# Optimization experiments

Measured on AMD Instinct MI355X. Metric: run time of the kernel, lower is better.

The kernel has to match this reference:

```python
import jax, jax.numpy as jnp
import numpy as np

N, E, D, G, L, ED = 20000, 640000, 128, 128, 5, 7
BN_EPS = 1e-5


def _bn(x, g, b):
    # training-mode BatchNorm1d: biased batch statistics
    m = x.mean(axis=0)
    v = jnp.mean((x - m) ** 2, axis=0)
    return g * (x - m) / jnp.sqrt(v + BN_EPS) + b


def setup_inputs() -> dict:
    key = jax.random.key(0)
    ks = jax.random.split(key, 16)
    s = 0.05
    p = {}
    p["x"] = jax.random.normal(ks[0], (N, D), jnp.float32)
    p["edge_attr"] = jax.random.normal(ks[1], (E, ED), jnp.float32)
    p["edge_index"] = jax.random.randint(ks[2], (2, E), 0, N, jnp.int32)
    p["batch"] = jnp.sort(jax.random.randint(ks[3], (N,), 0, G, jnp.int32))
    p["enc_W"] = jax.random.normal(ks[4], (D, D), jnp.float32) * s
    p["enc_b"] = jnp.zeros((D,), jnp.float32)
    p["vn_emb"] = jnp.zeros((1, D), jnp.float32)  # init.constant_(0)
    p["eps"] = jnp.zeros((L,), jnp.float32)       # GIN eps init 0
    p["edge_W"] = jax.random.normal(ks[5], (L, ED, D), jnp.float32) * s
    p["edge_b"] = jnp.zeros((L, D), jnp.float32)
    p["mlp_W1"] = jax.random.normal(ks[6], (L, D, 2 * D), jnp.float32) * s
    p["mlp_b1"] = jnp.zeros((L, 2 * D), jnp.float32)
    p["mlp_bn1_g"] = jnp.ones((L, 2 * D), jnp.float32)
    p["mlp_bn1_b"] = jnp.zeros((L, 2 * D), jnp.float32)
    p["mlp_W2"] = jax.random.normal(ks[7], (L, 2 * D, D), jnp.float32) * s
    p["mlp_b2"] = jnp.zeros((L, D), jnp.float32)
    p["bn_g"] = jnp.ones((L, D), jnp.float32)
    p["bn_b"] = jnp.zeros((L, D), jnp.float32)
    p["vn_W1"] = jax.random.normal(ks[8], (L - 1, D, 2 * D), jnp.float32) * s
    p["vn_b1"] = jnp.zeros((L - 1, 2 * D), jnp.float32)
    p["vn_bn1_g"] = jnp.ones((L - 1, 2 * D), jnp.float32)
    p["vn_bn1_b"] = jnp.zeros((L - 1, 2 * D), jnp.float32)
    p["vn_W2"] = jax.random.normal(ks[9], (L - 1, 2 * D, D), jnp.float32) * s
    p["vn_b2"] = jnp.zeros((L - 1, D), jnp.float32)
    p["vn_bn2_g"] = jnp.ones((L - 1, D), jnp.float32)
    p["vn_bn2_b"] = jnp.zeros((L - 1, D), jnp.float32)
    return p


def reference(x, edge_attr, edge_index, batch, enc_W, enc_b, vn_emb, eps,
              edge_W, edge_b, mlp_W1, mlp_b1, mlp_bn1_g, mlp_bn1_b, mlp_W2,
              mlp_b2, bn_g, bn_b, vn_W1, vn_b1, vn_bn1_g, vn_bn1_b, vn_W2,
              vn_b2, vn_bn2_g, vn_bn2_b):
    src, dst = edge_index[0], edge_index[1]
    h = x @ enc_W + enc_b                       # node_encoder (Linear)
    vn = jnp.broadcast_to(vn_emb[0], (G, D))    # virtual node per graph, init 0
    for l in range(L):
        h_in = h + vn[batch]                    # gather virtual node into nodes
        # GINConv: message = relu(x_j + edge_emb), aggr='add'
        eemb = edge_attr @ edge_W[l] + edge_b[l]            # [E, D]
        msg = jax.nn.relu(h_in[src] + eemb)                 # [E, D]
        agg = jax.ops.segment_sum(msg, dst, num_segments=N) # scatter-add
        z = (1.0 + eps[l]) * h_in + agg
        z = jax.nn.relu(_bn(z @ mlp_W1[l] + mlp_b1[l], mlp_bn1_g[l], mlp_bn1_b[l]))
        z = z @ mlp_W2[l] + mlp_b2[l]
        hn = _bn(z, bn_g[l], bn_b[l])           # outer BatchNorm1d
        if l < L - 1:
            hn = jax.nn.relu(hn)                # relu on all but last layer
            # virtual node update: global_add_pool over h_list[layer] (= h_in)
            pooled = jax.ops.segment_sum(h_in, batch, num_segments=G) + vn
            t = jax.nn.relu(_bn(pooled @ vn_W1[l] + vn_b1[l], vn_bn1_g[l], vn_bn1_b[l]))
            vn = jax.nn.relu(_bn(t @ vn_W2[l] + vn_b2[l], vn_bn2_g[l], vn_bn2_b[l]))
        h = hn
    return h  # JK='last' node representation [N, D]
```

## Files before the change

kernel.cpp:

```cpp
#include <hip/hip_runtime.h>

#define N_NODES 20000
#define N_EDGES 640000
#define DIM 128
#define NGRAPH 128
#define NLAYER 5
#define EDIM 7
#define TWO_D 256

typedef __bf16 bf16x8 __attribute__((ext_vector_type(8)));
typedef __bf16 bf16x4 __attribute__((ext_vector_type(4)));
typedef __bf16 bf16x2 __attribute__((ext_vector_type(2)));
typedef float  f32x4  __attribute__((ext_vector_type(4)));

__device__ __forceinline__ f32x4 mfma16(bf16x8 a, bf16x8 b, f32x4 c) {
  return __builtin_amdgcn_mfma_f32_16x16x32_bf16(a, b, c, 0, 0, 0);
}

__global__ void k_hist(const int* __restrict__ dst, int* __restrict__ counts) {
  int e = blockIdx.x * blockDim.x + threadIdx.x;
  if (e < N_EDGES) atomicAdd(&counts[dst[e]], 1);
}

__global__ __launch_bounds__(1024) void k_scanA(const int* __restrict__ counts,
    int* __restrict__ local, int* __restrict__ bsum) {
  __shared__ int sd[1024];
  int b = blockIdx.x, tid = threadIdx.x;
  int i = b * 1024 + tid;
  int v = (i < N_NODES) ? counts[i] : 0;
  sd[tid] = v;
  __syncthreads();
  for (int ofs = 1; ofs < 1024; ofs <<= 1) {
    int t = (tid >= ofs) ? sd[tid - ofs] : 0;
    __syncthreads();
    sd[tid] += t;
    __syncthreads();
  }
  if (i <= N_NODES) local[i] = sd[tid] - v;
  if (tid == 1023) bsum[b] = sd[1023];
}

__global__ void k_scanB(int* __restrict__ bsum, int* __restrict__ carry,
                        int* __restrict__ offsets, const int* __restrict__ batch,
                        int* __restrict__ gs) {
  int tid = threadIdx.x;
  if (tid == 0) {
    int run = 0;
    for (int b = 0; b < 20; ++b) { carry[b] = run; run += bsum[b]; }
    offsets[N_NODES] = run;
  }
  if (tid <= NGRAPH) {
    if (tid == NGRAPH) gs[NGRAPH] = N_NODES;
    else {
      int lo = 0, hi = N_NODES;
      while (lo < hi) { int mid = (lo + hi) >> 1; if (batch[mid] < tid) lo = mid + 1; else hi = mid; }
      gs[tid] = lo;
    }
  }
}

__global__ __launch_bounds__(1024) void k_scanC(const int* __restrict__ local,
    const int* __restrict__ carry, int* __restrict__ offsets) {
  int i = blockIdx.x * 1024 + threadIdx.x;
  if (i < N_NODES) offsets[i] = local[i] + carry[i >> 10];
}

__global__ void k_fillA(const int* __restrict__ dstArr, const int* __restrict__ offsets,
                        int* __restrict__ cursor, int* __restrict__ perm) {
  int e = blockIdx.x * blockDim.x + threadIdx.x;
  if (e >= N_EDGES) return;
  int d = dstArr[e];
  int p = offsets[d] + atomicAdd(&cursor[d], 1);
  perm[p] = e;
}

__global__ void k_fillB(const int* __restrict__ perm, const int* __restrict__ srcArr,
                        const float* __restrict__ edge_attr,
                        int* __restrict__ csr_src, __bf16* __restrict__ ea_csr) {
  int i = blockIdx.x * blockDim.x + threadIdx.x;
  if (i >= N_EDGES) return;
  int e = perm[i];
  csr_src[i] = srcArr[e];
  const float* ea = edge_attr + (size_t)e * EDIM;
  bf16x8 v;
#pragma unroll
  for (int k = 0; k < EDIM; ++k) v[k] = (__bf16)ea[k];
  v[7] = (__bf16)0.f;
  *(bf16x8*)(ea_csr + (size_t)i * 8) = v;
}

__global__ void k_convAll(const float* __restrict__ encW, const float* __restrict__ W1,
    const float* __restrict__ W2,
    __bf16* __restrict__ encT_hi, __bf16* __restrict__ encT_lo,
    __bf16* __restrict__ W1T_hi, __bf16* __restrict__ W1T_lo,
    __bf16* __restrict__ W2T_hi, __bf16* __restrict__ W2T_lo) {
  const int t1 = DIM * DIM;
  const int t2 = NLAYER * DIM * TWO_D;
  const int total = t1 + t2 + t2;
  for (int i = blockIdx.x * blockDim.x + threadIdx.x; i < total;
       i += gridDim.x * blockDim.x) {
    const float* src; __bf16 *dh, *dl; int K, C, idx;
    if (i < t1)            { src = encW; dh = encT_hi; dl = encT_lo; K = DIM;   C = DIM;   idx = i; }
    else if (i < t1 + t2)  { src = W1;   dh = W1T_hi;  dl = W1T_lo;  K = DIM;   C = TWO_D; idx = i - t1; }
    else                   { src = W2;   dh = W2T_hi;  dl = W2T_lo;  K = TWO_D; C = DIM;   idx = i - t1 - t2; }
    int l = idx / (K * C);
    int rem = idx - l * K * C;
    int k = rem / C;
    int c = rem - k * C;
    float v = src[idx];
    __bf16 hi = (__bf16)v;
    __bf16 lo = (__bf16)(v - (float)hi);
    size_t o = (size_t)l * K * C + (size_t)c * K + k;
    dh[o] = hi;
    dl[o] = lo;
  }
}

__global__ void k_vninit(const float* __restrict__ vn_emb, float* __restrict__ vn) {
  int i = blockIdx.x * blockDim.x + threadIdx.x;
  if (i < NGRAPH * DIM) vn[i] = vn_emb[i & (DIM - 1)];
}

__global__ __launch_bounds__(128) void k_enc(const float* __restrict__ x,
    const __bf16* __restrict__ encT_hi, const __bf16* __restrict__ encT_lo,
    const float* __restrict__ enc_b, const float* __restrict__ vn_emb,
    __bf16* __restrict__ h_hi, __bf16* __restrict__ h_lo) {
  int lane = threadIdx.x & 63, wid = threadIdx.x >> 6;
  int rbase = blockIdx.x * 32 + wid * 16;
  int r = rbase + (lane & 15);
  int ko = (lane >> 4) * 8;
  const float* xr = x + (size_t)r * DIM;
  bf16x8 a_hi[4], a_lo[4];
#pragma unroll
  for (int ks = 0; ks < 4; ++ks) {
    f32x4 v0 = *(const f32x4*)(xr + ks * 32 + ko);
    f32x4 v1 = *(const f32x4*)(xr + ks * 32 + ko + 4);
    bf16x8 th, tl;
#pragma unroll
    for (int j = 0; j < 4; ++j) {
      th[j] = (__bf16)v0[j];     tl[j] = (__bf16)(v0[j] - (float)th[j]);
      th[4+j] = (__bf16)v1[j];   tl[4+j] = (__bf16)(v1[j] - (float)th[4+j]);
    }
    a_hi[ks] = th; a_lo[ks] = tl;
  }
  const f32x4 fz = {0.f, 0.f, 0.f, 0.f};
  f32x4 acc[8];
#pragma unroll
  for (int nf = 0; nf < 8; ++nf) acc[nf] = fz;
#pragma unroll
  for (int nf = 0; nf < 8; ++nf) {
    size_t wrow = (size_t)(nf * 16 + (lane & 15)) * DIM + ko;
    const __bf16* bh = encT_hi + wrow;
    const __bf16* bl = encT_lo + wrow;
#pragma unroll
    for (int ks = 0; ks < 4; ++ks) {
      bf16x8 wh = *(const bf16x8*)(bh + ks * 32);
      bf16x8 wl = *(const bf16x8*)(bl + ks * 32);
      acc[nf] = mfma16(a_hi[ks], wh, acc[nf]);
      acc[nf] = mfma16(a_lo[ks], wh, acc[nf]);
      acc[nf] = mfma16(a_hi[ks], wl, acc[nf]);
    }
  }
  int c0 = lane & 15;
  int rr = rbase + (lane >> 4) * 4;
#pragma unroll
  for (int nf = 0; nf < 8; ++nf) {
    int c = nf * 16 + c0;
    float bias = enc_b[c] + vn_emb[c];
#pragma unroll
    for (int j = 0; j < 4; ++j) {
      float v = acc[nf][j] + bias;
      __bf16 hi = (__bf16)v;
      h_hi[(size_t)(rr + j) * DIM + c] = hi;
      h_lo[(size_t)(rr + j) * DIM + c] = (__bf16)(v - (float)hi);
    }
  }
}

__global__ __launch_bounds__(1024) void k_pool(const __bf16* __restrict__ h_hi,
    const int* __restrict__ gs, const float* __restrict__ vnbuf,
    const float* __restrict__ vnr, const float* __restrict__ sv2,
    const float* __restrict__ qv2, const float* __restrict__ bn2g,
    const float* __restrict__ bn2b, int use_stats,
    float* __restrict__ pooled) {
  __shared__ float red[8][DIM];
  __shared__ float vns[DIM];
  int tid = threadIdx.x;
  int g = blockIdx.x;
  if (tid < DIM) {
    if (use_stats) {
      float s = 0.f, q = 0.f;
#pragma unroll
      for (int rep = 0; rep < 8; ++rep) { s += sv2[rep * DIM + tid]; q += qv2[rep * DIM + tid]; }
      float m = s * (1.f / NGRAPH);
      float var = q * (1.f / NGRAPH) - m * m;
      float a = bn2g[tid] / sqrtf(var + 1e-5f);
      vns[tid] = fmaxf(vnr[g * DIM + tid] * a + (bn2b[tid] - m * a), 0.f);
    } else {
      vns[tid] = vnbuf[g * DIM + tid];
    }
  }
  __syncthreads();
  int d = tid & 127, slot = tid >> 7;
  int lo = gs[g], hi = gs[g + 1];
  float acc = 0.f;
  for (int n = lo + slot; n < hi; n += 8)
    acc += (float)h_hi[(size_t)n * DIM + d];
  red[slot][d] = acc;
  __syncthreads();
  if (slot == 0) {
    float t = vns[d];
#pragma unroll
    for (int s2 = 0; s2 < 8; ++s2) t += red[s2][d];
    pooled[g * DIM + d] = t;
  }
}

__global__ __launch_bounds__(256) void k_agg(const __bf16* __restrict__ h_hi,
    const __bf16* __restrict__ h_lo, const int* __restrict__ offsets,
    const int* __restrict__ csr_src, const __bf16* __restrict__ ea_csr,
    const float* __restrict__ eW, const float* __restrict__ eB,
    const float* __restrict__ eps, int l,
    __bf16* __restrict__ z_hi, __bf16* __restrict__ z_lo) {
  int tid = threadIdx.x;
  int lane = tid & 63, w = tid >> 6;
  int l2 = lane * 2;
  int n = blockIdx.x * 4 + w;
  float w0[EDIM], w1[EDIM];
#pragma unroll
  for (int k = 0; k < EDIM; ++k) {
    float2 wv = *(const float2*)(eW + k * DIM + l2);
    w0[k] = wv.x; w1[k] = wv.y;
  }
  float2 ebv = *(const float2*)(eB + l2);
  int off = offsets[n], end = offsets[n + 1];
  float acc0 = 0.f, acc1 = 0.f;

  auto edge = [&](int iu) {
    int s = csr_src[iu];
    const unsigned* eu = (const unsigned*)(ea_csr + (size_t)iu * 8);
    unsigned u0 = eu[0], u1 = eu[1], u2 = eu[2], u3 = eu[3];
    unsigned hv = *(const unsigned*)(h_hi + (size_t)s * DIM + l2);
    float e0 = __builtin_bit_cast(float, u0 << 16);
    float e1 = __builtin_bit_cast(float, u0 & 0xffff0000u);
    float e2 = __builtin_bit_cast(float, u1 << 16);
    float e3 = __builtin_bit_cast(float, u1 & 0xffff0000u);
    float e4 = __builtin_bit_cast(float, u2 << 16);
    float e5 = __builtin_bit_cast(float, u2 & 0xffff0000u);
    float e6 = __builtin_bit_cast(float, u3 << 16);
    float m0 = __builtin_bit_cast(float, hv << 16) + ebv.x;
    float m1 = __builtin_bit_cast(float, hv & 0xffff0000u) + ebv.y;
    m0 = fmaf(e0, w0[0], m0); m1 = fmaf(e0, w1[0], m1);
    m0 = fmaf(e1, w0[1], m0); m1 = fmaf(e1, w1[1], m1);
    m0 = fmaf(e2, w0[2], m0); m1 = fmaf(e2, w1[2], m1);
    m0 = fmaf(e3, w0[3], m0); m1 = fmaf(e3, w1[3], m1);
    m0 = fmaf(e4, w0[4], m0); m1 = fmaf(e4, w1[4], m1);
    m0 = fmaf(e5, w0[5], m0); m1 = fmaf(e5, w1[5], m1);
    m0 = fmaf(e6, w0[6], m0); m1 = fmaf(e6, w1[6], m1);
    acc0 += fmaxf(m0, 0.f);
    acc1 += fmaxf(m1, 0.f);
  };

  int i = off;
  for (; i + 3 < end; i += 4) {
    int iu = __builtin_amdgcn_readfirstlane(i);
    edge(iu);
    edge(iu + 1);
    edge(iu + 2);
    edge(iu + 3);
  }
  for (; i < end; ++i) {
    edge(__builtin_amdgcn_readfirstlane(i));
  }
  float epsv = 1.f + eps[l];
  unsigned hvh = *(const unsigned*)(h_hi + (size_t)n * DIM + l2);
  unsigned hvl = *(const unsigned*)(h_lo + (size_t)n * DIM + l2);
  float s0 = __builtin_bit_cast(float, hvh << 16) + __builtin_bit_cast(float, hvl << 16);
  float s1 = __builtin_bit_cast(float, hvh & 0xffff0000u) + __builtin_bit_cast(float, hvl & 0xffff0000u);
  float v0 = epsv * s0 + acc0;
  float v1 = epsv * s1 + acc1;
  __bf16 hi0 = (__bf16)v0, hi1 = (__bf16)v1;
  bf16x2 zh; zh[0] = hi0; zh[1] = hi1;
  bf16x2 zl; zl[0] = (__bf16)(v0 - (float)hi0); zl[1] = (__bf16)(v1 - (float)hi1);
  *(bf16x2*)(z_hi + (size_t)n * DIM + l2) = zh;
  *(bf16x2*)(z_lo + (size_t)n * DIM + l2) = zl;
}

__global__ __launch_bounds__(256) void k_gemm1(const __bf16* __restrict__ z_hi,
    const __bf16* __restrict__ z_lo,
    const __bf16* __restrict__ W1T_hi, const __bf16* __restrict__ W1T_lo,
    const float* __restrict__ b1,
    __bf16* __restrict__ y1h, __bf16* __restrict__ y1l,
    float* __restrict__ s1, float* __restrict__ q1) {
  int tid = threadIdx.x;
  int lane = tid & 63, wid = tid >> 6;
  int rowH = wid >> 1, colH = wid & 1;
  int rbase = blockIdx.x * 32 + rowH * 16;
  int r = rbase + (lane & 15);
  int ko = (lane >> 4) * 8;
  bf16x8 a_hi[4], a_lo[4];
#pragma unroll
  for (int ks = 0; ks < 4; ++ks) {
    a_hi[ks] = *(const bf16x8*)(z_hi + (size_t)r * DIM + ks * 32 + ko);
    a_lo[ks] = *(const bf16x8*)(z_lo + (size_t)r * DIM + ks * 32 + ko);
  }
  const f32x4 fz = {0.f, 0.f, 0.f, 0.f};
  f32x4 acc[8];
#pragma unroll
  for (int nf8 = 0; nf8 < 8; ++nf8) acc[nf8] = fz;
#pragma unroll
  for (int nf8 = 0; nf8 < 8; ++nf8) {
    int nf = colH * 8 + nf8;
    size_t wrow = (size_t)(nf * 16 + (lane & 15)) * DIM + ko;
    const __bf16* bh = W1T_hi + wrow;
    const __bf16* bl = W1T_lo + wrow;
#pragma unroll
    for (int ks = 0; ks < 4; ++ks) {
      bf16x8 wh = *(const bf16x8*)(bh + ks * 32);
      bf16x8 wl = *(const bf16x8*)(bl + ks * 32);
      acc[nf8] = mfma16(a_hi[ks], wh, acc[nf8]);
      acc[nf8] = mfma16(a_lo[ks], wh, acc[nf8]);
      acc[nf8] = mfma16(a_hi[ks], wl, acc[nf8]);
    }
  }
  int c0 = lane & 15;
  int rr = rbase + (lane >> 4) * 4;
  int rep = blockIdx.x & 7;
#pragma unroll
  for (int nf8 = 0; nf8 < 8; ++nf8) {
    int c = (colH * 8 + nf8) * 16 + c0;
    float bias = b1[c];
    float s = 0.f, q = 0.f;
#pragma unroll
    for (int j = 0; j < 4; ++j) {
      float v = acc[nf8][j] + bias;
      __bf16 hi = (__bf16)v;
      y1h[(size_t)(rr + j) * TWO_D + c] = hi;
      y1l[(size_t)(rr + j) * TWO_D + c] = (__bf16)(v - (float)hi);
      s += v; q += v * v;
    }
    s += __shfl_xor(s, 16); s += __shfl_xor(s, 32);
    q += __shfl_xor(q, 16); q += __shfl_xor(q, 32);
    if (lane < 16) {
      atomicAdd(&s1[rep * TWO_D + c], s);
      atomicAdd(&q1[rep * TWO_D + c], q);
    }
  }
}

__global__ __launch_bounds__(256) void k_gemm2(const __bf16* __restrict__ y1h,
    const __bf16* __restrict__ y1l,
    const __bf16* __restrict__ W2T_hi, const __bf16* __restrict__ W2T_lo,
    const float* __restrict__ b2,
    const float* __restrict__ s1, const float* __restrict__ q1,
    const float* __restrict__ bn1g, const float* __restrict__ bn1b,
    float* __restrict__ y2, float* __restrict__ s2, float* __restrict__ q2) {
  __shared__ float sc1s[TWO_D], sh1s[TWO_D];
  int tid = threadIdx.x;
  {
    int c = tid;
    float s = 0.f, q = 0.f;
#pragma unroll
    for (int rep = 0; rep < 8; ++rep) { s += s1[rep * TWO_D + c]; q += q1[rep * TWO_D + c]; }
    float m = s * (1.f / N_NODES);
    float var = q * (1.f / N_NODES) - m * m;
    float a = bn1g[c] / sqrtf(var + 1e-5f);
    sc1s[c] = a; sh1s[c] = bn1b[c] - m * a;
  }
  __syncthreads();
  int lane = tid & 63, wid = tid >> 6;
  int rowH = wid >> 1, colH = wid & 1;
  int rbase = blockIdx.x * 32 + rowH * 16;
  int r = rbase + (lane & 15);
  int ko = (lane >> 4) * 8;
  bf16x8 a_hi[8], a_lo[8];
#pragma unroll
  for (int ks = 0; ks < 8; ++ks) {
    int kb = ks * 32 + ko;
    bf16x8 rh = *(const bf16x8*)(y1h + (size_t)r * TWO_D + kb);
    bf16x8 rl = *(const bf16x8*)(y1l + (size_t)r * TWO_D + kb);
    f32x4 sc0 = *(const f32x4*)(&sc1s[kb]);
    f32x4 sc1 = *(const f32x4*)(&sc1s[kb + 4]);
    f32x4 sh0 = *(const f32x4*)(&sh1s[kb]);
    f32x4 sh1 = *(const f32x4*)(&sh1s[kb + 4]);
    bf16x8 th, tl;
#pragma unroll
    for (int j = 0; j < 4; ++j) {
      float r0 = (float)rh[j] + (float)rl[j];
      float r1 = (float)rh[4 + j] + (float)rl[4 + j];
      float v0 = fmaxf(r0 * sc0[j] + sh0[j], 0.f);
      float v1 = fmaxf(r1 * sc1[j] + sh1[j], 0.f);
      th[j] = (__bf16)v0;     tl[j] = (__bf16)(v0 - (float)th[j]);
      th[4+j] = (__bf16)v1;   tl[4+j] = (__bf16)(v1 - (float)th[4+j]);
    }
    a_hi[ks] = th; a_lo[ks] = tl;
  }
  const f32x4 fz = {0.f, 0.f, 0.f, 0.f};
  f32x4 acc[4];
#pragma unroll
  for (int nf4 = 0; nf4 < 4; ++nf4) acc[nf4] = fz;
#pragma unroll
  for (int nf4 = 0; nf4 < 4; ++nf4) {
    int nf = colH * 4 + nf4;
    size_t wrow = (size_t)(nf * 16 + (lane & 15)) * TWO_D + ko;
    const __bf16* bh = W2T_hi + wrow;
    const __bf16* bl = W2T_lo + wrow;
#pragma unroll
    for (int ks = 0; ks < 8; ++ks) {
      bf16x8 wh = *(const bf16x8*)(bh + ks * 32);
      bf16x8 wl = *(const bf16x8*)(bl + ks * 32);
      acc[nf4] = mfma16(a_hi[ks], wh, acc[nf4]);
      acc[nf4] = mfma16(a_lo[ks], wh, acc[nf4]);
      acc[nf4] = mfma16(a_hi[ks], wl, acc[nf4]);
    }
  }
  int c0 = lane & 15;
  int rr = rbase + (lane >> 4) * 4;
  int rep = blockIdx.x & 7;
#pragma unroll
  for (int nf4 = 0; nf4 < 4; ++nf4) {
    int c = (colH * 4 + nf4) * 16 + c0;
    float bias = b2[c];
    float s = 0.f, q = 0.f;
#pragma unroll
    for (int j = 0; j < 4; ++j) {
      float v = acc[nf4][j] + bias;
      y2[(size_t)(rr + j) * DIM + c] = v;
      s += v; q += v * v;
    }
    s += __shfl_xor(s, 16); s += __shfl_xor(s, 32);
    q += __shfl_xor(q, 16); q += __shfl_xor(q, 32);
    if (lane < 16) {
      atomicAdd(&s2[rep * DIM + c], s);
      atomicAdd(&q2[rep * DIM + c], q);
    }
  }
}

__global__ __launch_bounds__(256) void k_vgemm1(const float* __restrict__ pooled,
    const float* __restrict__ W1, const float* __restrict__ b1,
    float* __restrict__ tv, float* __restrict__ sv1, float* __restrict__ qv1) {
  __shared__ float row[DIM];
  int g = blockIdx.x, tid = threadIdx.x;
  if (tid < DIM) row[tid] = pooled[g * DIM + tid];
  __syncthreads();
  int c = tid;
  float acc = b1[c];
  for (int k = 0; k < DIM; ++k) acc = fmaf(row[k], W1[k * TWO_D + c], acc);
  tv[g * TWO_D + c] = acc;
  int rep = g & 7;
  atomicAdd(&sv1[rep * TWO_D + c], acc);
  atomicAdd(&qv1[rep * TWO_D + c], acc * acc);
}

__global__ __launch_bounds__(256) void k_vgemm2(const float* __restrict__ tv,
    const float* __restrict__ sv1, const float* __restrict__ qv1,
    const float* __restrict__ bn1g, const float* __restrict__ bn1b,
    const float* __restrict__ W2, const float* __restrict__ b2,
    float* __restrict__ vnr, float* __restrict__ sv2, float* __restrict__ qv2) {
  __shared__ float trow[TWO_D];
  int g = blockIdx.x, tid = threadIdx.x;
  {
    float s = 0.f, q = 0.f;
#pragma unroll
    for (int rep = 0; rep < 8; ++rep) { s += sv1[rep * TWO_D + tid]; q += qv1[rep * TWO_D + tid]; }
    float m = s * (1.f / NGRAPH);
    float var = q * (1.f / NGRAPH) - m * m;
    float a = bn1g[tid] / sqrtf(var + 1e-5f);
    trow[tid] = fmaxf(tv[g * TWO_D + tid] * a + (bn1b[tid] - m * a), 0.f);
  }
  __syncthreads();
  if (tid < DIM) {
    float acc = b2[tid];
    for (int k = 0; k < TWO_D; ++k) acc = fmaf(trow[k], W2[k * DIM + tid], acc);
    vnr[g * DIM + tid] = acc;
    int rep = g & 7;
    atomicAdd(&sv2[rep * DIM + tid], acc);
    atomicAdd(&qv2[rep * DIM + tid], acc * acc);
  }
}

__global__ __launch_bounds__(256) void k_bn2hin(const float* __restrict__ y2,
    const float* __restrict__ s2, const float* __restrict__ q2,
    const float* __restrict__ bng, const float* __restrict__ bnb,
    const float* __restrict__ vnr, const float* __restrict__ sv2,
    const float* __restrict__ qv2, const float* __restrict__ vbn2g,
    const float* __restrict__ vbn2b, const int* __restrict__ batch,
    __bf16* __restrict__ h_hi, __bf16* __restrict__ h_lo) {
  __shared__ float sc2s[DIM], sh2s[DIM], scvn[DIM], shvn[DIM];
  int tid = threadIdx.x;
  if (tid < DIM) {
    float s = 0.f, q = 0.f;
#pragma unroll
    for (int rep = 0; rep < 8; ++rep) { s += s2[rep * DIM + tid]; q += q2[rep * DIM + tid]; }
    float m = s * (1.f / N_NODES);
    float var = q * (1.f / N_NODES) - m * m;
    float a = bng[tid] / sqrtf(var + 1e-5f);
    sc2s[tid] = a; sh2s[tid] = bnb[tid] - m * a;
    float sv = 0.f, qv = 0.f;
#pragma unroll
    for (int rep = 0; rep < 8; ++rep) { sv += sv2[rep * DIM + tid]; qv += qv2[rep * DIM + tid]; }
    float mv = sv * (1.f / NGRAPH);
    float varv = qv * (1.f / NGRAPH) - mv * mv;
    float av = vbn2g[tid] / sqrtf(varv + 1e-5f);
    scvn[tid] = av; shvn[tid] = vbn2b[tid] - mv * av;
  }
  __syncthreads();
  int idx = blockIdx.x * 256 + tid;
  if (idx >= N_NODES * (DIM / 4)) return;
  int c4 = idx & 31;
  int row = idx >> 5;
  f32x4 y = ((const f32x4*)y2)[idx];
  f32x4 scv = ((const f32x4*)sc2s)[c4];
  f32x4 shv = ((const f32x4*)sh2s)[c4];
  f32x4 vsc = ((const f32x4*)scvn)[c4];
  f32x4 vsh = ((const f32x4*)shvn)[c4];
  int b = batch[row];
  f32x4 vr = ((const f32x4*)vnr)[b * 32 + c4];
  bf16x4 oh, ol;
#pragma unroll
  for (int j = 0; j < 4; ++j) {
    float vnv = fmaxf(vr[j] * vsc[j] + vsh[j], 0.f);
    float o = fmaxf(y[j] * scv[j] + shv[j], 0.f) + vnv;
    __bf16 hi = (__bf16)o;
    oh[j] = hi;
    ol[j] = (__bf16)(o - (float)hi);
  }
  ((bf16x4*)h_hi)[idx] = oh;
  ((bf16x4*)h_lo)[idx] = ol;
}

__global__ __launch_bounds__(256) void k_out(const float* __restrict__ y2,
    const float* __restrict__ s2, const float* __restrict__ q2,
    const float* __restrict__ bng, const float* __restrict__ bnb,
    float* __restrict__ out) {
  __shared__ float sc2s[DIM], sh2s[DIM];
  int tid = threadIdx.x;
  if (tid < DIM) {
    float s = 0.f, q = 0.f;
#pragma unroll
    for (int rep = 0; rep < 8; ++rep) { s += s2[rep * DIM + tid]; q += q2[rep * DIM + tid]; }
    float m = s * (1.f / N_NODES);
    float var = q * (1.f / N_NODES) - m * m;
    float a = bng[tid] / sqrtf(var + 1e-5f);
    sc2s[tid] = a; sh2s[tid] = bnb[tid] - m * a;
  }
  __syncthreads();
  int idx = blockIdx.x * 256 + tid;
  if (idx >= N_NODES * (DIM / 4)) return;
  int c4 = idx & 31;
  f32x4 y = ((const f32x4*)y2)[idx];
  f32x4 scv = ((const f32x4*)sc2s)[c4];
  f32x4 shv = ((const f32x4*)sh2s)[c4];
  f32x4 o;
#pragma unroll
  for (int j = 0; j < 4; ++j) o[j] = y[j] * scv[j] + shv[j];
  ((f32x4*)out)[idx] = o;
}

extern "C" void kernel_launch(void* const* d_in, const int* in_sizes, int n_in,
                              void* d_out, int out_size, void* d_ws, size_t ws_size,
                              hipStream_t stream) {
  const float* x         = (const float*)d_in[0];
  const float* edge_attr = (const float*)d_in[1];
  const int*   edge_index= (const int*)d_in[2];
  const int*   batch     = (const int*)d_in[3];
  const float* enc_W     = (const float*)d_in[4];
  const float* enc_b     = (const float*)d_in[5];
  const float* vn_emb    = (const float*)d_in[6];
  const float* eps       = (const float*)d_in[7];
  const float* edge_W    = (const float*)d_in[8];
  const float* edge_b    = (const float*)d_in[9];
  const float* mlp_W1    = (const float*)d_in[10];
  const float* mlp_b1    = (const float*)d_in[11];
  const float* mlp_bn1_g = (const float*)d_in[12];
  const float* mlp_bn1_b = (const float*)d_in[13];
  const float* mlp_W2    = (const float*)d_in[14];
  const float* mlp_b2    = (const float*)d_in[15];
  const float* bn_g      = (const float*)d_in[16];
  const float* bn_b      = (const float*)d_in[17];
  const float* vn_W1     = (const float*)d_in[18];
  const float* vn_b1     = (const float*)d_in[19];
  const float* vn_bn1_g  = (const float*)d_in[20];
  const float* vn_bn1_b  = (const float*)d_in[21];
  const float* vn_W2     = (const float*)d_in[22];
  const float* vn_b2     = (const float*)d_in[23];
  const float* vn_bn2_g  = (const float*)d_in[24];
  const float* vn_bn2_b  = (const float*)d_in[25];

  char* wsb = (char*)d_ws;
  size_t off = 0;
  auto take = [&](size_t bytes) -> void* {
    void* p = wsb + off;
    off += (bytes + 255) & ~(size_t)255;
    return p;
  };
  int*    counts  = (int*)take((size_t)2 * N_NODES * 4);
  int*    cursor  = counts + N_NODES;
  float*  stats   = (float*)take((size_t)NLAYER * 12288 * 4);
  __bf16* h_hi    = (__bf16*)take((size_t)N_NODES * DIM * 2);
  __bf16* h_lo    = (__bf16*)take((size_t)N_NODES * DIM * 2);
  float*  y2      = (float*)take((size_t)N_NODES * DIM * 4);
  __bf16* y1h     = (__bf16*)take((size_t)N_NODES * TWO_D * 2);
  __bf16* y1l     = (__bf16*)take((size_t)N_NODES * TWO_D * 2);
  __bf16* z_hi    = (__bf16*)take((size_t)N_NODES * DIM * 2);
  __bf16* z_lo    = (__bf16*)take((size_t)N_NODES * DIM * 2);
  int*    csr_src = (int*)take((size_t)N_EDGES * 4);
  __bf16* ea_csr  = (__bf16*)take((size_t)N_EDGES * 8 * 2);
  int*    perm    = (int*)take((size_t)N_EDGES * 4);
  int*    offsets = (int*)take((size_t)(N_NODES + 1) * 4);
  int*    slocal  = (int*)take((size_t)(N_NODES + 1024) * 4);
  int*    sbsum   = (int*)take(64 * 4);
  int*    scarry  = sbsum + 32;
  int*    gs      = (int*)take((size_t)(NGRAPH + 1) * 4);
  float*  pooled  = (float*)take((size_t)NGRAPH * DIM * 4);
  float*  tv      = (float*)take((size_t)NGRAPH * TWO_D * 4);
  float*  vnr     = (float*)take((size_t)NGRAPH * DIM * 4);
  float*  vn0     = (float*)take((size_t)NGRAPH * DIM * 4);
  __bf16* encT_hi = (__bf16*)take((size_t)DIM * DIM * 2);
  __bf16* encT_lo = (__bf16*)take((size_t)DIM * DIM * 2);
  __bf16* W1T_hi  = (__bf16*)take((size_t)NLAYER * DIM * TWO_D * 2);
  __bf16* W1T_lo  = (__bf16*)take((size_t)NLAYER * DIM * TWO_D * 2);
  __bf16* W2T_hi  = (__bf16*)take((size_t)NLAYER * TWO_D * DIM * 2);
  __bf16* W2T_lo  = (__bf16*)take((size_t)NLAYER * TWO_D * DIM * 2);
  if (off > ws_size) return;

  const int* srcArr = edge_index;
  const int* dstArr = edge_index + N_EDGES;

  hipMemsetAsync(counts, 0, (size_t)2 * N_NODES * 4 + (size_t)NLAYER * 12288 * 4, stream);

  k_hist<<<N_EDGES / 256, 256, 0, stream>>>(dstArr, counts);
  k_scanA<<<20, 1024, 0, stream>>>(counts, slocal, sbsum);
  k_scanB<<<1, 256, 0, stream>>>(sbsum, scarry, offsets, batch, gs);
  k_scanC<<<20, 1024, 0, stream>>>(slocal, scarry, offsets);
  k_fillA<<<N_EDGES / 256, 256, 0, stream>>>(dstArr, offsets, cursor, perm);
  k_fillB<<<N_EDGES / 256, 256, 0, stream>>>(perm, srcArr, edge_attr, csr_src, ea_csr);
  k_convAll<<<336, 1024, 0, stream>>>(enc_W, mlp_W1, mlp_W2,
      encT_hi, encT_lo, W1T_hi, W1T_lo, W2T_hi, W2T_lo);
  k_vninit<<<(NGRAPH * DIM) / 256, 256, 0, stream>>>(vn_emb, vn0);
  k_enc<<<N_NODES / 32, 128, 0, stream>>>(x, encT_hi, encT_lo, enc_b, vn_emb, h_hi, h_lo);

  for (int l = 0; l < NLAYER; ++l) {
    float* s1  = stats + (size_t)l * 12288;
    float* q1  = s1 + 2048;
    float* s2  = s1 + 4096;
    float* q2  = s1 + 5120;
    float* sv1 = s1 + 6144;
    float* qv1 = s1 + 8192;
    float* sv2 = s1 + 10240;
    float* qv2 = s1 + 11264;
    if (l < NLAYER - 1) {
      if (l == 0)
        k_pool<<<NGRAPH, 1024, 0, stream>>>(h_hi, gs, vn0, vn0, nullptr, nullptr,
            nullptr, nullptr, 0, pooled);
      else {
        float* psv2 = stats + (size_t)(l - 1) * 12288 + 10240;
        float* pqv2 = stats + (size_t)(l - 1) * 12288 + 11264;
        k_pool<<<NGRAPH, 1024, 0, stream>>>(h_hi, gs, vn0, vnr, psv2, pqv2,
            vn_bn2_g + (size_t)(l - 1) * DIM, vn_bn2_b + (size_t)(l - 1) * DIM, 1, pooled);
      }
    }
    k_agg<<<N_NODES / 4, 256, 0, stream>>>(h_hi, h_lo, offsets, csr_src, ea_csr,
        edge_W + (size_t)l * EDIM * DIM, edge_b + (size_t)l * DIM, eps, l, z_hi, z_lo);
    k_gemm1<<<N_NODES / 32, 256, 0, stream>>>(z_hi, z_lo,
        W1T_hi + (size_t)l * DIM * TWO_D, W1T_lo + (size_t)l * DIM * TWO_D,
        mlp_b1 + (size_t)l * TWO_D, y1h, y1l, s1, q1);
    k_gemm2<<<N_NODES / 32, 256, 0, stream>>>(y1h, y1l,
        W2T_hi + (size_t)l * TWO_D * DIM, W2T_lo + (size_t)l * TWO_D * DIM,
        mlp_b2 + (size_t)l * DIM, s1, q1,
        mlp_bn1_g + (size_t)l * TWO_D, mlp_bn1_b + (size_t)l * TWO_D,
        y2, s2, q2);
    if (l < NLAYER - 1) {
      k_vgemm1<<<NGRAPH, 256, 0, stream>>>(pooled, vn_W1 + (size_t)l * DIM * TWO_D,
          vn_b1 + (size_t)l * TWO_D, tv, sv1, qv1);
      k_vgemm2<<<NGRAPH, 256, 0, stream>>>(tv, sv1, qv1,
          vn_bn1_g + (size_t)l * TWO_D, vn_bn1_b + (size_t)l * TWO_D,
          vn_W2 + (size_t)l * TWO_D * DIM, vn_b2 + (size_t)l * DIM,
          vnr, sv2, qv2);
      k_bn2hin<<<(N_NODES * 32) / 256, 256, 0, stream>>>(y2, s2, q2,
          bn_g + (size_t)l * DIM, bn_b + (size_t)l * DIM,
          vnr, sv2, qv2, vn_bn2_g + (size_t)l * DIM, vn_bn2_b + (size_t)l * DIM,
          batch, h_hi, h_lo);
    } else {
      k_out<<<(N_NODES * 32) / 256, 256, 0, stream>>>(y2, s2, q2,
          bn_g + (size_t)l * DIM, bn_b + (size_t)l * DIM, (float*)d_out);
    }
  }
}
```

Before: 740.5 us.

## Fuse graph pooling into producer kernels via atomics; process two nodes per wave in agg

Removes the separate k_pool and k_vninit kernels. Per-graph sums of h_in are now accumulated with float atomics into 8 replicated partial buffers inside k_enc and k_bn2hin, and the virtual-node term is added in k_vgemm1. k_agg now handles two destination nodes per wave with interleaved edge loops, which adds memory-level parallelism. The price is many atomic adds (one per element, into 8 replicas), a larger memset of the pooled buffers, and nondeterministic float summation order. Pooling now sums the fp32 value rather than only the bf16 hi part.

```diff
diff --git a/kernel.cpp b/kernel.cpp
--- a/kernel.cpp
+++ b/kernel.cpp
@@ -116,15 +116,12 @@
   }
 }
 
-__global__ void k_vninit(const float* __restrict__ vn_emb, float* __restrict__ vn) {
-  int i = blockIdx.x * blockDim.x + threadIdx.x;
-  if (i < NGRAPH * DIM) vn[i] = vn_emb[i & (DIM - 1)];
-}
-
 __global__ __launch_bounds__(128) void k_enc(const float* __restrict__ x,
     const __bf16* __restrict__ encT_hi, const __bf16* __restrict__ encT_lo,
     const float* __restrict__ enc_b, const float* __restrict__ vn_emb,
-    __bf16* __restrict__ h_hi, __bf16* __restrict__ h_lo) {
+    const int* __restrict__ batch,
+    __bf16* __restrict__ h_hi, __bf16* __restrict__ h_lo,
+    float* __restrict__ pooled0) {
   int lane = threadIdx.x & 63, wid = threadIdx.x >> 6;
   int rbase = blockIdx.x * 32 + wid * 16;
   int r = rbase + (lane & 15);
@@ -163,6 +160,10 @@
   }
   int c0 = lane & 15;
   int rr = rbase + (lane >> 4) * 4;
+  int bj[4];
+#pragma unroll
+  for (int j = 0; j < 4; ++j) bj[j] = batch[rr + j];
+  float* prep = pooled0 + (size_t)(blockIdx.x & 7) * NGRAPH * DIM;
 #pragma unroll
   for (int nf = 0; nf < 8; ++nf) {
     int c = nf * 16 + c0;
@@ -173,46 +174,8 @@
       __bf16 hi = (__bf16)v;
       h_hi[(size_t)(rr + j) * DIM + c] = hi;
       h_lo[(size_t)(rr + j) * DIM + c] = (__bf16)(v - (float)hi);
-    }
-  }
-}
-
-__global__ __launch_bounds__(1024) void k_pool(const __bf16* __restrict__ h_hi,
-    const int* __restrict__ gs, const float* __restrict__ vnbuf,
-    const float* __restrict__ vnr, const float* __restrict__ sv2,
-    const float* __restrict__ qv2, const float* __restrict__ bn2g,
-    const float* __restrict__ bn2b, int use_stats,
-    float* __restrict__ pooled) {
-  __shared__ float red[8][DIM];
-  __shared__ float vns[DIM];
-  int tid = threadIdx.x;
-  int g = blockIdx.x;
-  if (tid < DIM) {
-    if (use_stats) {
-      float s = 0.f, q = 0.f;
-#pragma unroll
-      for (int rep = 0; rep < 8; ++rep) { s += sv2[rep * DIM + tid]; q += qv2[rep * DIM + tid]; }
-      float m = s * (1.f / NGRAPH);
-      float var = q * (1.f / NGRAPH) - m * m;
-      float a = bn2g[tid] / sqrtf(var + 1e-5f);
-      vns[tid] = fmaxf(vnr[g * DIM + tid] * a + (bn2b[tid] - m * a), 0.f);
-    } else {
-      vns[tid] = vnbuf[g * DIM + tid];
-    }
-  }
-  __syncthreads();
-  int d = tid & 127, slot = tid >> 7;
-  int lo = gs[g], hi = gs[g + 1];
-  float acc = 0.f;
-  for (int n = lo + slot; n < hi; n += 8)
-    acc += (float)h_hi[(size_t)n * DIM + d];
-  red[slot][d] = acc;
-  __syncthreads();
-  if (slot == 0) {
-    float t = vns[d];
-#pragma unroll
-    for (int s2 = 0; s2 < 8; ++s2) t += red[s2][d];
-    pooled[g * DIM + d] = t;
+      atomicAdd(&prep[bj[j] * DIM + c], v);
+    }
   }
 }
 
@@ -225,7 +188,8 @@
   int tid = threadIdx.x;
   int lane = tid & 63, w = tid >> 6;
   int l2 = lane * 2;
-  int n = blockIdx.x * 4 + w;
+  int n0 = blockIdx.x * 8 + w * 2;
+  int n1 = n0 + 1;
   float w0[EDIM], w1[EDIM];
 #pragma unroll
   for (int k = 0; k < EDIM; ++k) {
@@ -233,10 +197,11 @@
     w0[k] = wv.x; w1[k] = wv.y;
   }
   float2 ebv = *(const float2*)(eB + l2);
-  int off = offsets[n], end = offsets[n + 1];
-  float acc0 = 0.f, acc1 = 0.f;
-
-  auto edge = [&](int iu) {
+  int i0 = offsets[n0], e0_ = offsets[n0 + 1];
+  int i1 = e0_, e1_ = offsets[n1 + 1];
+  float a00 = 0.f, a01 = 0.f, a10 = 0.f, a11 = 0.f;
+
+  auto edge = [&](int iu, float& ax, float& ay) {
     int s = csr_src[iu];
     const unsigned* eu = (const unsigned*)(ea_csr + (size_t)iu * 8);
     unsigned u0 = eu[0], u1 = eu[1], u2 = eu[2], u3 = eu[3];
@@ -257,33 +222,40 @@
     m0 = fmaf(e4, w0[4], m0); m1 = fmaf(e4, w1[4], m1);
     m0 = fmaf(e5, w0[5], m0); m1 = fmaf(e5, w1[5], m1);
     m0 = fmaf(e6, w0[6], m0); m1 = fmaf(e6, w1[6], m1);
-    acc0 += fmaxf(m0, 0.f);
-    acc1 += fmaxf(m1, 0.f);
+    ax += fmaxf(m0, 0.f);
+    ay += fmaxf(m1, 0.f);
   };
 
-  int i = off;
-  for (; i + 3 < end; i += 4) {
-    int iu = __builtin_amdgcn_readfirstlane(i);
-    edge(iu);
-    edge(iu + 1);
-    edge(iu + 2);
-    edge(iu + 3);
-  }
-  for (; i < end; ++i) {
-    edge(__builtin_amdgcn_readfirstlane(i));
-  }
+  while (i0 + 1 < e0_ && i1 + 1 < e1_) {
+    int u0 = __builtin_amdgcn_readfirstlane(i0);
+    int u1 = __builtin_amdgcn_readfirstlane(i1);
+    edge(u0, a00, a01);
+    edge(u1, a10, a11);
+    edge(u0 + 1, a00, a01);
+    edge(u1 + 1, a10, a11);
+    i0 += 2; i1 += 2;
+  }
+  for (; i0 < e0_; ++i0) edge(__builtin_amdgcn_readfirstlane(i0), a00, a01);
+  for (; i1 < e1_; ++i1) edge(__builtin_amdgcn_readfirstlane(i1), a10, a11);
+
   float epsv = 1.f + eps[l];
-  unsigned hvh = *(const unsigned*)(h_hi + (size_t)n * DIM + l2);
-  unsigned hvl = *(const unsigned*)(h_lo + (size_t)n * DIM + l2);
-  float s0 = __builtin_bit_cast(float, hvh << 16) + __builtin_bit_cast(float, hvl << 16);
-  float s1 = __builtin_bit_cast(float, hvh & 0xffff0000u) + __builtin_bit_cast(float, hvl & 0xffff0000u);
-  float v0 = epsv * s0 + acc0;
-  float v1 = epsv * s1 + acc1;
-  __bf16 hi0 = (__bf16)v0, hi1 = (__bf16)v1;
-  bf16x2 zh; zh[0] = hi0; zh[1] = hi1;
-  bf16x2 zl; zl[0] = (__bf16)(v0 - (float)hi0); zl[1] = (__bf16)(v1 - (float)hi1);
-  *(bf16x2*)(z_hi + (size_t)n * DIM + l2) = zh;
-  *(bf16x2*)(z_lo + (size_t)n * DIM + l2) = zl;
+#pragma unroll
+  for (int t = 0; t < 2; ++t) {
+    int n = (t == 0) ? n0 : n1;
+    float ax = (t == 0) ? a00 : a10;
+    float ay = (t == 0) ? a01 : a11;
+    unsigned hvh = *(const unsigned*)(h_hi + (size_t)n * DIM + l2);
+    unsigned hvl = *(const unsigned*)(h_lo + (size_t)n * DIM + l2);
+    float s0 = __builtin_bit_cast(float, hvh << 16) + __builtin_bit_cast(float, hvl << 16);
+    float s1 = __builtin_bit_cast(float, hvh & 0xffff0000u) + __builtin_bit_cast(float, hvl & 0xffff0000u);
+    float v0 = epsv * s0 + ax;
+    float v1 = epsv * s1 + ay;
+    __bf16 hi0 = (__bf16)v0, hi1 = (__bf16)v1;
+    bf16x2 zh; zh[0] = hi0; zh[1] = hi1;
+    bf16x2 zl; zl[0] = (__bf16)(v0 - (float)hi0); zl[1] = (__bf16)(v1 - (float)hi1);
+    *(bf16x2*)(z_hi + (size_t)n * DIM + l2) = zh;
+    *(bf16x2*)(z_lo + (size_t)n * DIM + l2) = zl;
+  }
 }
 
 __global__ __launch_bounds__(256) void k_gemm1(const __bf16* __restrict__ z_hi,
@@ -438,11 +410,31 @@
 }
 
 __global__ __launch_bounds__(256) void k_vgemm1(const float* __restrict__ pooled,
+    const float* __restrict__ vn_emb, const float* __restrict__ vnr,
+    const float* __restrict__ sv2p, const float* __restrict__ qv2p,
+    const float* __restrict__ vbn2g, const float* __restrict__ vbn2b, int use_stats,
     const float* __restrict__ W1, const float* __restrict__ b1,
     float* __restrict__ tv, float* __restrict__ sv1, float* __restrict__ qv1) {
   __shared__ float row[DIM];
   int g = blockIdx.x, tid = threadIdx.x;
-  if (tid < DIM) row[tid] = pooled[g * DIM + tid];
+  if (tid < DIM) {
+    float vnterm;
+    if (use_stats) {
+      float s = 0.f, q = 0.f;
+#pragma unroll
+      for (int rep = 0; rep < 8; ++rep) { s += sv2p[rep * DIM + tid]; q += qv2p[rep * DIM + tid]; }
+      float m = s * (1.f / NGRAPH);
+      float var = q * (1.f / NGRAPH) - m * m;
+      float a = vbn2g[tid] / sqrtf(var + 1e-5f);
+      vnterm = fmaxf(vnr[g * DIM + tid] * a + (vbn2b[tid] - m * a), 0.f);
+    } else {
+      vnterm = vn_emb[tid];
+    }
+    float ps = 0.f;
+#pragma unroll
+    for (int rep = 0; rep < 8; ++rep) ps += pooled[(size_t)rep * NGRAPH * DIM + g * DIM + tid];
+    row[tid] = ps + vnterm;
+  }
   __syncthreads();
   int c = tid;
   float acc = b1[c];
@@ -486,7 +478,8 @@
     const float* __restrict__ vnr, const float* __restrict__ sv2,
     const float* __restrict__ qv2, const float* __restrict__ vbn2g,
     const float* __restrict__ vbn2b, const int* __restrict__ batch,
-    __bf16* __restrict__ h_hi, __bf16* __restrict__ h_lo) {
+    __bf16* __restrict__ h_hi, __bf16* __restrict__ h_lo,
+    float* __restrict__ pooledNext) {
   __shared__ float sc2s[DIM], sh2s[DIM], scvn[DIM], shvn[DIM];
   int tid = threadIdx.x;
   if (tid < DIM) {
@@ -517,6 +510,7 @@
   f32x4 vsh = ((const f32x4*)shvn)[c4];
   int b = batch[row];
   f32x4 vr = ((const f32x4*)vnr)[b * 32 + c4];
+  float* prep = pooledNext + (size_t)(blockIdx.x & 7) * NGRAPH * DIM + (size_t)b * DIM + c4 * 4;
   bf16x4 oh, ol;
 #pragma unroll
   for (int j = 0; j < 4; ++j) {
@@ -525,6 +519,7 @@
     __bf16 hi = (__bf16)o;
     oh[j] = hi;
     ol[j] = (__bf16)(o - (float)hi);
+    atomicAdd(&prep[j], o);
   }
   ((bf16x4*)h_hi)[idx] = oh;
   ((bf16x4*)h_lo)[idx] = ol;
@@ -595,9 +590,13 @@
     off += (bytes + 255) & ~(size_t)255;
     return p;
   };
+  const size_t POOLED_LAYER = (size_t)8 * NGRAPH * DIM;
   int*    counts  = (int*)take((size_t)2 * N_NODES * 4);
   int*    cursor  = counts + N_NODES;
   float*  stats   = (float*)take((size_t)NLAYER * 12288 * 4);
+  float*  pooledL = (float*)take((size_t)NLAYER * POOLED_LAYER * 4);
+  size_t  memset_bytes = (size_t)2 * N_NODES * 4 + (size_t)NLAYER * 12288 * 4
+                       + (size_t)NLAYER * POOLED_LAYER * 4;
   __bf16* h_hi    = (__bf16*)take((size_t)N_NODES * DIM * 2);
   __bf16* h_lo    = (__bf16*)take((size_t)N_NODES * DIM * 2);
   float*  y2      = (float*)take((size_t)N_NODES * DIM * 4);
@@ -613,10 +612,8 @@
   int*    sbsum   = (int*)take(64 * 4);
   int*    scarry  = sbsum + 32;
   int*    gs      = (int*)take((size_t)(NGRAPH + 1) * 4);
-  float*  pooled  = (float*)take((size_t)NGRAPH * DIM * 4);
   float*  tv      = (float*)take((size_t)NGRAPH * TWO_D * 4);
   float*  vnr     = (float*)take((size_t)NGRAPH * DIM * 4);
-  float*  vn0     = (float*)take((size_t)NGRAPH * DIM * 4);
   __bf16* encT_hi = (__bf16*)take((size_t)DIM * DIM * 2);
   __bf16* encT_lo = (__bf16*)take((size_t)DIM * DIM * 2);
   __bf16* W1T_hi  = (__bf16*)take((size_t)NLAYER * DIM * TWO_D * 2);
@@ -628,7 +625,7 @@
   const int* srcArr = edge_index;
   const int* dstArr = edge_index + N_EDGES;
 
-  hipMemsetAsync(counts, 0, (size_t)2 * N_NODES * 4 + (size_t)NLAYER * 12288 * 4, stream);
+  hipMemsetAsync(counts, 0, memset_bytes, stream);
 
   k_hist<<<N_EDGES / 256, 256, 0, stream>>>(dstArr, counts);
   k_scanA<<<20, 1024, 0, stream>>>(counts, slocal, sbsum);
@@ -638,8 +635,8 @@
   k_fillB<<<N_EDGES / 256, 256, 0, stream>>>(perm, srcArr, edge_attr, csr_src, ea_csr);
   k_convAll<<<336, 1024, 0, stream>>>(enc_W, mlp_W1, mlp_W2,
       encT_hi, encT_lo, W1T_hi, W1T_lo, W2T_hi, W2T_lo);
-  k_vninit<<<(NGRAPH * DIM) / 256, 256, 0, stream>>>(vn_emb, vn0);
-  k_enc<<<N_NODES / 32, 128, 0, stream>>>(x, encT_hi, encT_lo, enc_b, vn_emb, h_hi, h_lo);
+  k_enc<<<N_NODES / 32, 128, 0, stream>>>(x, encT_hi, encT_lo, enc_b, vn_emb,
+      batch, h_hi, h_lo, pooledL);
 
   for (int l = 0; l < NLAYER; ++l) {
     float* s1  = stats + (size_t)l * 12288;
@@ -650,18 +647,7 @@
     float* qv1 = s1 + 8192;
     float* sv2 = s1 + 10240;
     float* qv2 = s1 + 11264;
-    if (l < NLAYER - 1) {
-      if (l == 0)
-        k_pool<<<NGRAPH, 1024, 0, stream>>>(h_hi, gs, vn0, vn0, nullptr, nullptr,
-            nullptr, nullptr, 0, pooled);
-      else {
-        float* psv2 = stats + (size_t)(l - 1) * 12288 + 10240;
-        float* pqv2 = stats + (size_t)(l - 1) * 12288 + 11264;
-        k_pool<<<NGRAPH, 1024, 0, stream>>>(h_hi, gs, vn0, vnr, psv2, pqv2,
-            vn_bn2_g + (size_t)(l - 1) * DIM, vn_bn2_b + (size_t)(l - 1) * DIM, 1, pooled);
-      }
-    }
-    k_agg<<<N_NODES / 4, 256, 0, stream>>>(h_hi, h_lo, offsets, csr_src, ea_csr,
+    k_agg<<<N_NODES / 8, 256, 0, stream>>>(h_hi, h_lo, offsets, csr_src, ea_csr,
         edge_W + (size_t)l * EDIM * DIM, edge_b + (size_t)l * DIM, eps, l, z_hi, z_lo);
     k_gemm1<<<N_NODES / 32, 256, 0, stream>>>(z_hi, z_lo,
         W1T_hi + (size_t)l * DIM * TWO_D, W1T_lo + (size_t)l * DIM * TWO_D,
@@ -672,8 +658,15 @@
         mlp_bn1_g + (size_t)l * TWO_D, mlp_bn1_b + (size_t)l * TWO_D,
         y2, s2, q2);
     if (l < NLAYER - 1) {
-      k_vgemm1<<<NGRAPH, 256, 0, stream>>>(pooled, vn_W1 + (size_t)l * DIM * TWO_D,
-          vn_b1 + (size_t)l * TWO_D, tv, sv1, qv1);
+      const float* psv2 = (l == 0) ? nullptr : stats + (size_t)(l - 1) * 12288 + 10240;
+      const float* pqv2 = (l == 0) ? nullptr : stats + (size_t)(l - 1) * 12288 + 11264;
+      k_vgemm1<<<NGRAPH, 256, 0, stream>>>(pooledL + (size_t)l * POOLED_LAYER,
+          vn_emb, vnr, psv2, pqv2,
+          (l == 0) ? nullptr : vn_bn2_g + (size_t)(l - 1) * DIM,
+          (l == 0) ? nullptr : vn_bn2_b + (size_t)(l - 1) * DIM,
+          (l == 0) ? 0 : 1,
+          vn_W1 + (size_t)l * DIM * TWO_D, vn_b1 + (size_t)l * TWO_D,
+          tv, sv1, qv1);
       k_vgemm2<<<NGRAPH, 256, 0, stream>>>(tv, sv1, qv1,
           vn_bn1_g + (size_t)l * TWO_D, vn_bn1_b + (size_t)l * TWO_D,
           vn_W2 + (size_t)l * TWO_D * DIM, vn_b2 + (size_t)l * DIM,
@@ -681,7 +674,7 @@
       k_bn2hin<<<(N_NODES * 32) / 256, 256, 0, stream>>>(y2, s2, q2,
           bn_g + (size_t)l * DIM, bn_b + (size_t)l * DIM,
           vnr, sv2, qv2, vn_bn2_g + (size_t)l * DIM, vn_bn2_b + (size_t)l * DIM,
-          batch, h_hi, h_lo);
+          batch, h_hi, h_lo, pooledL + (size_t)(l + 1) * POOLED_LAYER);
     } else {
       k_out<<<(N_NODES * 32) / 256, 256, 0, stream>>>(y2, s2, q2,
           bn_g + (size_t)l * DIM, bn_b + (size_t)l * DIM, (float*)d_out);
```

After: 1.004 ms. +35.6%, slower.
